# Kernel optimization log

Measured on AMD Instinct MI355X. Metric: run time of the kernel, lower is better.

The kernel has to match this reference:

```python
import jax, jax.numpy as jnp
import numpy as np

EPS = 1e-5
K_GROUP = 8  # k_group_size


def setup_inputs() -> dict:
    key = jax.random.key(0)
    ks = jax.random.split(key, 8)
    C = 384  # encoder_channel
    rn = lambda k, s: (jax.random.normal(k, s, dtype=jnp.float32) * 0.05)
    return {
        "point_groups": jax.random.normal(ks[0], (4, 256, 32, 3), dtype=jnp.float32),
        # first_conv: Conv1d(3,128,1)+BN+ReLU+Conv1d(128,256,1)
        "W1": rn(ks[1], (128, 3)), "b1": jnp.zeros(128, jnp.float32),
        "gamma1": jnp.ones(128, jnp.float32), "beta1": jnp.zeros(128, jnp.float32),
        "W2": rn(ks[2], (256, 128)), "b2": jnp.zeros(256, jnp.float32),
        # second_conv: Conv1d(512,512,1)+BN+ReLU+Conv1d(512,C,1)
        "W3": rn(ks[3], (512, 512)), "b3": jnp.zeros(512, jnp.float32),
        "gamma3": jnp.ones(512, jnp.float32), "beta3": jnp.zeros(512, jnp.float32),
        "W4": rn(ks[4], (C, 512)), "b4": jnp.zeros(C, jnp.float32),
        # K_Norm affine (out_dim = C, matching declared parameter shapes)
        "alpha": jnp.ones((1, 1, 1, C), jnp.float32),
        "beta_aff": jnp.zeros((1, 1, 1, C), jnp.float32),
        # fusion_layer: Conv1d(2C,C,1)+BN+ReLU
        "Wf": rn(ks[5], (C, 2 * C)), "bf": jnp.zeros(C, jnp.float32),
        "gammaf": jnp.ones(C, jnp.float32), "betaf": jnp.zeros(C, jnp.float32),
    }


def _conv1x1(x, W, b):  # x: (B,Cin,L), W: (Cout,Cin)
    return jnp.einsum("bcl,oc->bol", x, W) + b[None, :, None]


def _bn(x, gamma, beta):  # training-mode BatchNorm1d over (batch, length)
    mu = jnp.mean(x, axis=(0, 2), keepdims=True)
    var = jnp.var(x, axis=(0, 2), keepdims=True)
    xh = (x - mu) * jax.lax.rsqrt(var + EPS)
    return xh * gamma[None, :, None] + beta[None, :, None]


def reference(point_groups, W1, b1, gamma1, beta1, W2, b2, W3, b3, gamma3, beta3,
              W4, b4, alpha, beta_aff, Wf, bf, gammaf, betaf):
    bs, g, n, _ = point_groups.shape
    C = W4.shape[0]
    pg = point_groups.reshape(bs * g, n, 3)  # (B', n, 3)

    # first_conv stack
    f = _conv1x1(pg.transpose(0, 2, 1), W1, b1)           # (B',128,n)
    f = jax.nn.relu(_bn(f, gamma1, beta1))
    f = _conv1x1(f, W2, b2)                               # (B',256,n)
    fg = jnp.max(f, axis=2, keepdims=True)                # (B',256,1)
    f = jnp.concatenate([jnp.broadcast_to(fg, f.shape), f], axis=1)  # (B',512,n)

    # second_conv stack
    f = _conv1x1(f, W3, b3)
    f = jax.nn.relu(_bn(f, gamma3, beta3))
    f = _conv1x1(f, W4, b4)                               # (B',C,n)
    feat = f.transpose(0, 2, 1)                           # (B',n,C)

    # KNN within each group (self included, as in KNN(xyz,xyz))
    sq = jnp.sum(pg * pg, axis=-1)                        # (B',n)
    d = sq[:, :, None] + sq[:, None, :] - 2.0 * jnp.einsum("bnc,bmc->bnm", pg, pg)
    _, idx = jax.lax.top_k(-d, K_GROUP)                   # (B',n,K)

    gather = jax.vmap(lambda a, i: a[i])
    knn_x = gather(feat, idx)                             # (B',n,K,C)

    # K_Norm: center-relative normalization by global scalar std (torch.std, ddof=1)
    mean_x = feat[:, :, None, :]
    dx = knn_x - mean_x
    std_x = jnp.std(dx, ddof=1)
    knn_x = dx / (std_x + EPS)
    knn_x = alpha * knn_x + beta_aff                      # (B',n,K,C)

    enhanced = jnp.mean(knn_x, axis=2)                    # mean over K -> (B',n,C)
    enhanced = jnp.mean(enhanced, axis=1)                 # pool over n -> (B',C)

    fg2 = jnp.max(f, axis=2)                              # (B',C)
    fused_in = jnp.concatenate([fg2, enhanced], axis=1)[:, :, None]  # (B',2C,1)
    fused = jax.nn.relu(_bn(_conv1x1(fused_in, Wf, bf), gammaf, betaf))[:, :, 0]
    return fused.reshape(bs, g, C)
```

## Files before the change

kernel.cpp:

```cpp
#include <hip/hip_runtime.h>
#include <math.h>

#define EPS 1e-5f

typedef __attribute__((ext_vector_type(8))) short s16x8;
typedef __attribute__((ext_vector_type(4))) float f32x4;

__device__ __forceinline__ unsigned short f2bf(float x) {
    unsigned u = __float_as_uint(x);
    u += 0x7fffu + ((u >> 16) & 1u);
    return (unsigned short)(u >> 16);
}
__device__ __forceinline__ float bf2f(unsigned short h) {
    return __uint_as_float(((unsigned)h) << 16);
}
__device__ __forceinline__ unsigned long long pack4bf(float a, float b, float c, float d) {
    return (unsigned long long)f2bf(a)
         | ((unsigned long long)f2bf(b) << 16)
         | ((unsigned long long)f2bf(c) << 32)
         | ((unsigned long long)f2bf(d) << 48);
}

template<int CTRL>
__device__ __forceinline__ float dppmov(float x) {
    return __int_as_float(__builtin_amdgcn_update_dpp(
        0, __float_as_int(x), CTRL, 0xF, 0xF, true));
}
__device__ __forceinline__ float red16_sum(float x) {
    x += dppmov<0xB1>(x);
    x += dppmov<0x4E>(x);
    x += dppmov<0x141>(x);
    x += dppmov<0x140>(x);
    return x;
}
__device__ __forceinline__ float red16_max(float x) {
    x = fmaxf(x, dppmov<0xB1>(x));
    x = fmaxf(x, dppmov<0x4E>(x));
    x = fmaxf(x, dppmov<0x141>(x));
    x = fmaxf(x, dppmov<0x140>(x));
    return x;
}

__global__ __launch_bounds__(128) void k1_conv1_knn(
    const float* __restrict__ pg, const float* __restrict__ W1,
    const float* __restrict__ b1,
    const float* __restrict__ W2, const float* __restrict__ W3,
    const float* __restrict__ W4, const float* __restrict__ Wf,
    unsigned short* __restrict__ h1b,
    float* __restrict__ p1sb, float* __restrict__ p1qb,
    int* __restrict__ idxw,
    unsigned short* __restrict__ W2b, unsigned short* __restrict__ W3b,
    unsigned short* __restrict__ W4b, unsigned short* __restrict__ Wfb)
{
    __shared__ float pgs[96];
    __shared__ float sqs[32];
    if (blockIdx.x >= 1024) {
        const int i = (blockIdx.x - 1024) * 128 + threadIdx.x;
        if (i < 32768)  W2b[i] = f2bf(W2[i]);
        if (i < 262144) W3b[i] = f2bf(W3[i]);
        if (i < 196608) W4b[i] = f2bf(W4[i]);
        if (i < 294912) Wfb[i] = f2bf(Wf[i]);
        return;
    }
    const int b = blockIdx.x;
    const int t = threadIdx.x;
    if (t < 96) pgs[t] = pg[b * 96 + t];
    __syncthreads();
    if (t < 32) {
        float x = pgs[t*3+0], y = pgs[t*3+1], z = pgs[t*3+2];
        sqs[t] = x*x + y*y + z*z;
    }
    __syncthreads();
    {
        const float w0 = W1[t*3+0], w1 = W1[t*3+1], w2 = W1[t*3+2];
        const float bb = b1[t];
        float s = 0.f, q = 0.f;
        unsigned short* hcol = h1b + (size_t)b*4096 + t;
        #pragma unroll
        for (int l = 0; l < 32; ++l) {
            float v = fmaf(w2, pgs[l*3+2], fmaf(w1, pgs[l*3+1], fmaf(w0, pgs[l*3+0], bb)));
            hcol[l*128] = f2bf(v); s += v; q += v*v;
        }
        atomicAdd(&p1sb[((b & 7) << 7) + t], s);
        atomicAdd(&p1qb[((b & 7) << 7) + t], q);
    }
    if (t < 32) {
        const float xl = pgs[t*3+0], yl = pgs[t*3+1], zl = pgs[t*3+2];
        const float sql = sqs[t];
        float dist[32];
        #pragma unroll
        for (int m = 0; m < 32; ++m) {
            float dot = xl*pgs[m*3+0] + yl*pgs[m*3+1] + zl*pgs[m*3+2];
            dist[m] = sql + sqs[m] - 2.f*dot;
        }
        unsigned used = 0u;
        int* orow = idxw + b*256 + t*8;
        #pragma unroll
        for (int j = 0; j < 8; ++j) {
            float best = 3.4e38f; int bi = 0;
            #pragma unroll
            for (int m = 0; m < 32; ++m) {
                if (!((used >> m) & 1u) && dist[m] < best) { best = dist[m]; bi = m; }
            }
            used |= (1u << bi);
            orow[j] = bi;
        }
    }
}

__global__ __launch_bounds__(1024, 8) void k3_mfma(
    const unsigned short* __restrict__ h1b,
    const float* __restrict__ gamma1, const float* __restrict__ beta1,
    const float* __restrict__ p1sb, const float* __restrict__ p1qb,
    const unsigned short* __restrict__ W2b, const float* __restrict__ b2,
    const unsigned short* __restrict__ W3b, const float* __restrict__ b3,
    unsigned short* __restrict__ h3b,
    float* __restrict__ p3sb, float* __restrict__ p3qb)
{
    const int g0 = blockIdx.x * 2;
    const int t = threadIdx.x;
    __shared__ __align__(16) unsigned short SB[26128];
    unsigned short* B1  = SB;
    unsigned short* F2  = SB + 8704;
    unsigned short* FGB = SB + 25600;
    __shared__ __align__(16) float sc1s[128], sh1s[128];

    if (t < 128) {
        float S = 0.f, Q = 0.f;
        #pragma unroll
        for (int bb = 0; bb < 8; ++bb) {
            S += p1sb[(bb << 7) + t];
            Q += p1qb[(bb << 7) + t];
        }
        float mu  = S * (1.f/32768.f);
        float var = Q * (1.f/32768.f) - mu*mu;
        float sc  = gamma1[t] * rsqrtf(var + EPS);
        sc1s[t] = sc;
        sh1s[t] = beta1[t] - mu * sc;
    }
    __syncthreads();

    {
        const int l = t >> 4, c0 = (t & 15) * 8;
        const int g = g0 + (l >> 5);
        s16x8 hv = *(const s16x8*)(h1b + (size_t)g*4096 + (l & 31)*128 + c0);
        unsigned short ov[8];
        #pragma unroll
        for (int e = 0; e < 8; ++e) {
            int c = c0 + e;
            float v = fmaxf(fmaf(bf2f((unsigned short)hv[e]), sc1s[c], sh1s[c]), 0.f);
            ov[e] = f2bf(v);
        }
        uint4 o4;
        o4.x = (unsigned)ov[0] | ((unsigned)ov[1] << 16);
        o4.y = (unsigned)ov[2] | ((unsigned)ov[3] << 16);
        o4.z = (unsigned)ov[4] | ((unsigned)ov[5] << 16);
        o4.w = (unsigned)ov[6] | ((unsigned)ov[7] << 16);
        *(uint4*)&B1[l*136 + c0] = o4;
    }
    __syncthreads();

    const int wave = t >> 6;
    const int lane = t & 63;
    const int m    = lane & 15;
    const int quad = lane >> 4;

    f32x4 acc2[4];
    #pragma unroll
    for (int n = 0; n < 4; ++n)
        acc2[n] = (f32x4){0.f, 0.f, 0.f, 0.f};

    #pragma unroll
    for (int kt = 0; kt < 4; ++kt) {
        s16x8 bv[4];
        #pragma unroll
        for (int nt = 0; nt < 4; ++nt)
            bv[nt] = *(const s16x8*)&B1[(nt*16 + m)*136 + kt*32 + quad*8];
        s16x8 av = *(const s16x8*)(W2b + (size_t)(wave*16 + m)*128 + kt*32 + quad*8);
        #pragma unroll
        for (int nt = 0; nt < 4; ++nt)
            acc2[nt] = __builtin_amdgcn_mfma_f32_16x16x32_bf16(av, bv[nt], acc2[nt], 0, 0, 0);
    }

    {
        const int o0 = wave*16 + quad*4;
        #pragma unroll
        for (int r = 0; r < 4; ++r) {
            float bb = b2[o0 + r];
            #pragma unroll
            for (int nt = 0; nt < 4; ++nt) acc2[nt][r] += bb;
        }
        #pragma unroll
        for (int nt = 0; nt < 4; ++nt) {
            const int row = nt*16 + m;
            *(unsigned long long*)&F2[row*264 + o0] =
                pack4bf(acc2[nt][0], acc2[nt][1], acc2[nt][2], acc2[nt][3]);
        }
        float f0[4], f1[4];
        #pragma unroll
        for (int r = 0; r < 4; ++r) {
            f0[r] = red16_max(fmaxf(acc2[0][r], acc2[1][r]));
            f1[r] = red16_max(fmaxf(acc2[2][r], acc2[3][r]));
        }
        if (m == 0) {
            *(unsigned long long*)&FGB[o0]       = pack4bf(f0[0], f0[1], f0[2], f0[3]);
            *(unsigned long long*)&FGB[264 + o0] = pack4bf(f1[0], f1[1], f1[2], f1[3]);
        }
    }
    __syncthreads();

    unsigned short* dst = h3b + (size_t)blockIdx.x * 32768;
    const int binbase = (blockIdx.x & 7) << 9;
    #pragma unroll
    for (int mt = 0; mt < 2; ++mt) {
        const int ot = wave*2 + mt;
        const int o0 = ot*16 + quad*4;

        f32x4 facc = (f32x4){0.f, 0.f, 0.f, 0.f};
        #pragma unroll
        for (int kt = 0; kt < 8; ++kt) {
            s16x8 bg = *(const s16x8*)&FGB[(m & 1)*264 + kt*32 + quad*8];
            s16x8 av = *(const s16x8*)(W3b + (size_t)(ot*16 + m)*512 + kt*32 + quad*8);
            facc = __builtin_amdgcn_mfma_f32_16x16x32_bf16(av, bg, facc, 0, 0, 0);
        }

        f32x4 acc3[4];
        #pragma unroll
        for (int r = 0; r < 4; ++r) {
            float self = facc[r];
            float oth  = dppmov<0xB1>(self);
            float fg_g0 = (m & 1) ? oth : self;
            float fg_g1 = (m & 1) ? self : oth;
            float bb = b3[o0 + r];
            acc3[0][r] = bb + fg_g0;
            acc3[1][r] = bb + fg_g0;
            acc3[2][r] = bb + fg_g1;
            acc3[3][r] = bb + fg_g1;
        }

        #pragma unroll
        for (int kt = 0; kt < 8; ++kt) {
            s16x8 bv[4];
            #pragma unroll
            for (int nt = 0; nt < 4; ++nt)
                bv[nt] = *(const s16x8*)&F2[(nt*16 + m)*264 + kt*32 + quad*8];
            s16x8 av = *(const s16x8*)(W3b + (size_t)(ot*16 + m)*512 + 256 + kt*32 + quad*8);
            #pragma unroll
            for (int nt = 0; nt < 4; ++nt)
                acc3[nt] = __builtin_amdgcn_mfma_f32_16x16x32_bf16(av, bv[nt], acc3[nt], 0, 0, 0);
        }

        float s[4], q[4];
        #pragma unroll
        for (int r = 0; r < 4; ++r) {
            float x0 = acc3[0][r], x1 = acc3[1][r];
            float x2 = acc3[2][r], x3 = acc3[3][r];
            s[r] = (x0 + x1) + (x2 + x3);
            q[r] = (x0*x0 + x1*x1) + (x2*x2 + x3*x3);
        }
        {
            unsigned long long u0 = pack4bf(acc3[0][0], acc3[0][1], acc3[0][2], acc3[0][3]);
            unsigned long long u1 = pack4bf(acc3[1][0], acc3[1][1], acc3[1][2], acc3[1][3]);
            unsigned long long u2 = pack4bf(acc3[2][0], acc3[2][1], acc3[2][2], acc3[2][3]);
            unsigned long long u3 = pack4bf(acc3[3][0], acc3[3][1], acc3[3][2], acc3[3][3]);
            unsigned short* p = dst + (size_t)(ot*64 + lane) * 16;
            *(uint4*)(p)     = make_uint4((unsigned)u0, (unsigned)(u0 >> 32), (unsigned)u1, (unsigned)(u1 >> 32));
            *(uint4*)(p + 8) = make_uint4((unsigned)u2, (unsigned)(u2 >> 32), (unsigned)u3, (unsigned)(u3 >> 32));
        }
        #pragma unroll
        for (int r = 0; r < 4; ++r) {
            s[r] = red16_sum(s[r]);
            q[r] = red16_sum(q[r]);
        }
        if (m == 0) {
            #pragma unroll
            for (int r = 0; r < 4; ++r) {
                atomicAdd(&p3sb[binbase + o0 + r], s[r]);
                atomicAdd(&p3qb[binbase + o0 + r], q[r]);
            }
        }
    }
}

__global__ __launch_bounds__(512, 4) void k5_mfma(
    const unsigned short* __restrict__ h3b,
    const float* __restrict__ gamma3, const float* __restrict__ beta3,
    const float* __restrict__ p3sb, const float* __restrict__ p3qb,
    const unsigned short* __restrict__ W4b, const float* __restrict__ b4,
    const int* __restrict__ idxw,
    float* __restrict__ fg2, float* __restrict__ A,
    float* __restrict__ S1p, float* __restrict__ S2p)
{
    const int g0 = blockIdx.x * 2;
    const int t = threadIdx.x;
    __shared__ __align__(16) unsigned short SB[33280];
    unsigned short* B4 = SB;
    unsigned short* XT = SB;
    unsigned short* Mm = SB + 30720;
    __shared__ __align__(16) float sc3s[512], sh3s[512];
    __shared__ int icnt[2][32];
    __shared__ float r1[2][8], r2[2][8];

    {
        float S = 0.f, Q = 0.f;
        #pragma unroll
        for (int bb = 0; bb < 8; ++bb) {
            S += p3sb[(bb << 9) + t];
            Q += p3qb[(bb << 9) + t];
        }
        float mu  = S * (1.f/32768.f);
        float var = Q * (1.f/32768.f) - mu*mu;
        float sc  = gamma3[t] * rsqrtf(var + EPS);
        sc3s[t] = sc;
        sh3s[t] = beta3[t] - mu * sc;
    }
    if (t < 64) icnt[t >> 5][t & 31] = 0;
    __syncthreads();

    {
        const uint4* src = (const uint4*)(h3b + (size_t)blockIdx.x * 32768);
        for (int i = t; i < 4096; i += 512) {
            uint4 hv = src[i];
            const int flat16 = i >> 1, half = i & 1;
            const int ln = flat16 & 63, m2 = ln & 15, q2 = ln >> 4;
            const int wm = flat16 >> 6;
            const int o0 = wm*16 + q2*4;
            const float4 sc = *(const float4*)&sc3s[o0];
            const float4 sh = *(const float4*)&sh3s[o0];
            const int rowa = (half*2)*16 + m2;
            float a0 = fmaxf(fmaf(bf2f((unsigned short)(hv.x       )), sc.x, sh.x), 0.f);
            float a1 = fmaxf(fmaf(bf2f((unsigned short)(hv.x >> 16 )), sc.y, sh.y), 0.f);
            float a2 = fmaxf(fmaf(bf2f((unsigned short)(hv.y       )), sc.z, sh.z), 0.f);
            float a3 = fmaxf(fmaf(bf2f((unsigned short)(hv.y >> 16 )), sc.w, sh.w), 0.f);
            float b0 = fmaxf(fmaf(bf2f((unsigned short)(hv.z       )), sc.x, sh.x), 0.f);
            float b1 = fmaxf(fmaf(bf2f((unsigned short)(hv.z >> 16 )), sc.y, sh.y), 0.f);
            float b2 = fmaxf(fmaf(bf2f((unsigned short)(hv.w       )), sc.z, sh.z), 0.f);
            float b3 = fmaxf(fmaf(bf2f((unsigned short)(hv.w >> 16 )), sc.w, sh.w), 0.f);
            *(unsigned long long*)&B4[rowa*520 + o0]        = pack4bf(a0, a1, a2, a3);
            *(unsigned long long*)&B4[(rowa + 16)*520 + o0] = pack4bf(b0, b1, b2, b3);
        }
    }
    __syncthreads();

    const int wave = t >> 6;
    const int lane = t & 63;
    const int m    = lane & 15;
    const int quad = lane >> 4;

    f32x4 acc4[3][4];
    #pragma unroll
    for (int mt = 0; mt < 3; ++mt)
        #pragma unroll
        for (int n = 0; n < 4; ++n)
            acc4[mt][n] = (f32x4){0.f, 0.f, 0.f, 0.f};

    #pragma unroll 4
    for (int kt = 0; kt < 16; ++kt) {
        s16x8 bv[4];
        #pragma unroll
        for (int nt = 0; nt < 4; ++nt)
            bv[nt] = *(const s16x8*)&B4[(nt*16 + m)*520 + kt*32 + quad*8];
        #pragma unroll
        for (int mt = 0; mt < 3; ++mt) {
            s16x8 av = *(const s16x8*)(W4b + (size_t)(wave*48 + mt*16 + m)*512 + kt*32 + quad*8);
            #pragma unroll
            for (int nt = 0; nt < 4; ++nt)
                acc4[mt][nt] = __builtin_amdgcn_mfma_f32_16x16x32_bf16(av, bv[nt], acc4[mt][nt], 0, 0, 0);
        }
    }

    #pragma unroll
    for (int mt = 0; mt < 3; ++mt) {
        const int o0 = wave*48 + mt*16 + quad*4;
        float f0[4], f1[4];
        #pragma unroll
        for (int r = 0; r < 4; ++r) {
            float bb = b4[o0 + r];
            #pragma unroll
            for (int nt = 0; nt < 4; ++nt) acc4[mt][nt][r] += bb;
            f0[r] = red16_max(fmaxf(acc4[mt][0][r], acc4[mt][1][r]));
            f1[r] = red16_max(fmaxf(acc4[mt][2][r], acc4[mt][3][r]));
        }
        if (m == 0) {
            #pragma unroll
            for (int r = 0; r < 4; ++r) {
                fg2[(size_t)g0*384 + o0 + r]     = f0[r];
                fg2[(size_t)(g0+1)*384 + o0 + r] = f1[r];
            }
        }
    }
    __syncthreads();

    #pragma unroll
    for (int mt = 0; mt < 3; ++mt) {
        const int o0 = wave*48 + mt*16 + quad*4;
        #pragma unroll
        for (int nt = 0; nt < 4; ++nt) {
            const int g = nt >> 1;
            const int l = (nt & 1)*16 + m;
            unsigned short* xg = XT + g*15360;
            #pragma unroll
            for (int r = 0; r < 4; ++r)
                xg[(o0 + r)*40 + l] = f2bf(acc4[mt][nt][r]);
        }
    }
    if (t < 64) {
        const int g = t >> 5, l = t & 31;
        uint4 z = make_uint4(0u, 0u, 0u, 0u);
        #pragma unroll
        for (int i = 0; i < 5; ++i)
            *(uint4*)&Mm[g*1280 + l*40 + i*8] = z;
    }
    __syncthreads();

    if (t < 64) {
        const int g = t >> 5, l = t & 31;
        const int* ip = idxw + (size_t)(g0 + g)*256 + l*8;
        #pragma unroll
        for (int j = 0; j < 8; ++j) {
            int ix = ip[j];
            Mm[g*1280 + l*40 + ix] = 0x3F80;
            atomicAdd(&icnt[g][ix], 1);
        }
    }
    __syncthreads();

    float s1loc[2] = {0.f, 0.f}, s2loc[2] = {0.f, 0.f};
    #pragma unroll
    for (int g = 0; g < 2; ++g) {
        const float c0 = (float)icnt[g][m];
        const float c1 = (float)icnt[g][m + 16];
        const float w0 = c0 - 8.f, u0 = c0 + 8.f;
        const float w1 = c1 - 8.f, u1 = c1 + 8.f;
        #pragma unroll
        for (int mt = 0; mt < 3; ++mt) {
            const int o0 = wave*48 + mt*16 + quad*4;
            float Ap[4];
            #pragma unroll
            for (int r = 0; r < 4; ++r) {
                const float x0 = acc4[mt][g*2 + 0][r];
                const float x1 = acc4[mt][g*2 + 1][r];
                Ap[r] = w0*x0 + w1*x1;
                s1loc[g] += Ap[r];
                s2loc[g] += u0*x0*x0 + u1*x1*x1;
            }
            #pragma unroll
            for (int r = 0; r < 4; ++r)
                Ap[r] = red16_sum(Ap[r]);
            if (m == 0) {
                #pragma unroll
                for (int r = 0; r < 4; ++r)
                    A[(size_t)(g0 + g)*384 + o0 + r] = Ap[r];
            }
        }
    }

    #pragma unroll
    for (int g = 0; g < 2; ++g) {
        const unsigned short* xg = XT + g*15360;
        float cross = 0.f;
        #pragma unroll
        for (int lt = 0; lt < 2; ++lt) {
            s16x8 af = *(const s16x8*)&Mm[g*1280 + (lt*16 + m)*40 + quad*8];
            #pragma unroll
            for (int i = 0; i < 3; ++i) {
                const int oc = (wave*3 + i)*16 + m;
                s16x8 bfv = *(const s16x8*)&xg[oc*40 + quad*8];
                f32x4 sa = __builtin_amdgcn_mfma_f32_16x16x32_bf16(
                    af, bfv, (f32x4){0.f, 0.f, 0.f, 0.f}, 0, 0, 0);
                #pragma unroll
                for (int r = 0; r < 4; ++r) {
                    const int lp = lt*16 + quad*4 + r;
                    cross = fmaf(bf2f(xg[oc*40 + lp]), sa[r], cross);
                }
            }
        }
        s2loc[g] -= 2.f * cross;
    }

    #pragma unroll
    for (int g = 0; g < 2; ++g) {
        float sA = s1loc[g], sQ = s2loc[g];
        #pragma unroll
        for (int off = 32; off > 0; off >>= 1) {
            sA += __shfl_down(sA, off, 64);
            sQ += __shfl_down(sQ, off, 64);
        }
        if (lane == 0) { r1[g][wave] = sA; r2[g][wave] = sQ; }
    }
    __syncthreads();
    if (t < 2) {
        float S = 0.f, Q = 0.f;
        #pragma unroll
        for (int w = 0; w < 8; ++w) { S += r1[t][w]; Q += r2[t][w]; }
        S1p[g0 + t] = S;
        S2p[g0 + t] = Q;
    }
}

__global__ __launch_bounds__(384) void k7_fused(
    const float* __restrict__ fg2, const float* __restrict__ A,
    const float* __restrict__ alpha, const float* __restrict__ beta_aff,
    const float* __restrict__ S1p, const float* __restrict__ S2p,
    const unsigned short* __restrict__ Wfb, const float* __restrict__ bf,
    float* __restrict__ hf, float* __restrict__ pfs, float* __restrict__ pfq)
{
    const int blk    = blockIdx.x;
    const int slice  = blk >> 2;
    const int msplit = blk & 3;
    const int g0     = slice * 16;
    const int obase  = msplit * 96;
    const int t = threadIdx.x;
    __shared__ __align__(16) char smem[24832];
    unsigned short* xfb = (unsigned short*)smem;
    float* OTf = (float*)smem;
    __shared__ double rs[6], rq[6];
    __shared__ float stdsh;

    {
        double s = 0.0, q = 0.0;
        for (int i = t; i < 1024; i += 384) { s += (double)S1p[i]; q += (double)S2p[i]; }
        #pragma unroll
        for (int off = 32; off > 0; off >>= 1) {
            s += __shfl_down(s, off, 64);
            q += __shfl_down(q, off, 64);
        }
        if ((t & 63) == 0) { rs[t >> 6] = s; rq[t >> 6] = q; }
        __syncthreads();
        if (t == 0) {
            double S = 0.0, Q = 0.0;
            #pragma unroll
            for (int w = 0; w < 6; ++w) { S += rs[w]; Q += rq[w]; }
            const double N = 1024.0 * 32.0 * 8.0 * 384.0;
            double var = (Q - S*S/N) / (N - 1.0);
            stdsh = (float)sqrt(var);
        }
        __syncthreads();
    }
    const float inv = 1.f / (256.f * (stdsh + EPS));

    for (int i = t; i < 16*96; i += 384) {
        const int row = i / 96, c8 = (i % 96) * 8;
        const int g = g0 + row;
        float e[8];
        if (c8 < 384) {
            const float4* s0 = (const float4*)(fg2 + (size_t)g*384 + c8);
            float4 v0 = s0[0], v1 = s0[1];
            e[0]=v0.x; e[1]=v0.y; e[2]=v0.z; e[3]=v0.w;
            e[4]=v1.x; e[5]=v1.y; e[6]=v1.z; e[7]=v1.w;
        } else {
            const int cc = c8 - 384;
            const float4* s0 = (const float4*)(A + (size_t)g*384 + cc);
            float4 v0 = s0[0], v1 = s0[1];
            float av[8] = {v0.x,v0.y,v0.z,v0.w,v1.x,v1.y,v1.z,v1.w};
            #pragma unroll
            for (int j = 0; j < 8; ++j)
                e[j] = fmaf(alpha[cc+j] * inv, av[j], beta_aff[cc+j]);
        }
        uint4 o4;
        o4.x = (unsigned)f2bf(e[0]) | ((unsigned)f2bf(e[1]) << 16);
        o4.y = (unsigned)f2bf(e[2]) | ((unsigned)f2bf(e[3]) << 16);
        o4.z = (unsigned)f2bf(e[4]) | ((unsigned)f2bf(e[5]) << 16);
        o4.w = (unsigned)f2bf(e[6]) | ((unsigned)f2bf(e[7]) << 16);
        *(uint4*)&xfb[row*776 + c8] = o4;
    }
    __syncthreads();

    const int wave = t >> 6;
    const int lane = t & 63;
    const int m    = lane & 15;
    const int quad = lane >> 4;

    f32x4 acc = (f32x4){0.f, 0.f, 0.f, 0.f};
    #pragma unroll 4
    for (int kt = 0; kt < 24; ++kt) {
        s16x8 bv = *(const s16x8*)&xfb[m*776 + kt*32 + quad*8];
        s16x8 av = *(const s16x8*)(Wfb + (size_t)(obase + wave*16 + m)*768 + kt*32 + quad*8);
        acc = __builtin_amdgcn_mfma_f32_16x16x32_bf16(av, bv, acc, 0, 0, 0);
    }

    {
        const int o0 = obase + wave*16 + quad*4;
        float s[4], q[4];
        #pragma unroll
        for (int r = 0; r < 4; ++r) {
            acc[r] += bf[o0 + r];
            s[r] = red16_sum(acc[r]);
            q[r] = red16_sum(acc[r]*acc[r]);
        }
        if (m == 0) {
            #pragma unroll
            for (int r = 0; r < 4; ++r) {
                pfs[(size_t)slice*384 + o0 + r] = s[r];
                pfq[(size_t)slice*384 + o0 + r] = q[r];
            }
        }
    }
    __syncthreads();

    {
        const int lo0 = wave*16 + quad*4;
        #pragma unroll
        for (int r = 0; r < 4; ++r)
            OTf[m*100 + lo0 + r] = acc[r];
    }
    __syncthreads();

    {
        const int grp = t / 24, c4 = t % 24;
        float4 v = *(const float4*)&OTf[grp*100 + c4*4];
        *(float4*)(hf + (size_t)(g0 + grp)*384 + obase + c4*4) = v;
    }
}

__global__ __launch_bounds__(384) void k9_out(
    const float* __restrict__ hf,
    const float* __restrict__ pfs, const float* __restrict__ pfq,
    const float* __restrict__ gammaf, const float* __restrict__ betaf,
    float* __restrict__ out)
{
    const int blk = blockIdx.x, t = threadIdx.x;
    float S = 0.f, Q = 0.f;
    #pragma unroll 8
    for (int i = 0; i < 64; ++i) {
        S += pfs[(size_t)i*384 + t];
        Q += pfq[(size_t)i*384 + t];
    }
    const float mu  = S * (1.f/1024.f);
    const float var = Q * (1.f/1024.f) - mu*mu;
    const float sc  = gammaf[t] * rsqrtf(var + EPS);
    const float sh  = betaf[t] - mu * sc;
    const size_t base = (size_t)blk * 8 * 384;
    #pragma unroll
    for (int g = 0; g < 8; ++g) {
        float v = fmaf(hf[base + g*384 + t], sc, sh);
        out[base + g*384 + t] = fmaxf(v, 0.f);
    }
}

extern "C" void kernel_launch(void* const* d_in, const int* in_sizes, int n_in,
                              void* d_out, int out_size, void* d_ws, size_t ws_size,
                              hipStream_t stream) {
    const float* pg      = (const float*)d_in[0];
    const float* W1      = (const float*)d_in[1];
    const float* b1      = (const float*)d_in[2];
    const float* gamma1  = (const float*)d_in[3];
    const float* beta1   = (const float*)d_in[4];
    const float* W2      = (const float*)d_in[5];
    const float* b2      = (const float*)d_in[6];
    const float* W3      = (const float*)d_in[7];
    const float* b3      = (const float*)d_in[8];
    const float* gamma3  = (const float*)d_in[9];
    const float* beta3   = (const float*)d_in[10];
    const float* W4      = (const float*)d_in[11];
    const float* b4      = (const float*)d_in[12];
    const float* alpha   = (const float*)d_in[13];
    const float* beta_af = (const float*)d_in[14];
    const float* Wf      = (const float*)d_in[15];
    const float* bf      = (const float*)d_in[16];
    const float* gammaf  = (const float*)d_in[17];
    const float* betaf   = (const float*)d_in[18];
    float* out = (float*)d_out;

    float* w = (float*)d_ws;
    unsigned short* h1b = (unsigned short*)w; w += 1024*4096/2;
    unsigned short* h3b = (unsigned short*)w; w += 1024*16384/2;
    unsigned short* W2b = (unsigned short*)w; w += 32768/2;
    unsigned short* W3b = (unsigned short*)w; w += 262144/2;
    unsigned short* W4b = (unsigned short*)w; w += 196608/2;
    unsigned short* Wfb = (unsigned short*)w; w += 294912/2;
    float* hf     = w;  w += 1024*384;
    float* fg2    = w;  w += 1024*384;
    float* A      = w;  w += 1024*384;
    float* p1sb   = w;  w += 8*128;
    float* p1qb   = w;  w += 8*128;
    float* p3sb   = w;  w += 8*512;
    float* p3qb   = w;  w += 8*512;
    float* pfs    = w;  w += 64*384;
    float* pfq    = w;  w += 64*384;
    float* S1p    = w;  w += 1024;
    float* S2p    = w;  w += 1024;
    int*   idxw   = (int*)w;  w += 1024*256;

    hipMemsetAsync(p1sb, 0, (8*128*2 + 8*512*2) * sizeof(float), stream);
    hipLaunchKernelGGL(k1_conv1_knn, dim3(1024 + 2304), dim3(128), 0, stream,
                       pg, W1, b1, W2, W3, W4, Wf,
                       h1b, p1sb, p1qb, idxw, W2b, W3b, W4b, Wfb);
    hipLaunchKernelGGL(k3_mfma, dim3(512), dim3(1024), 0, stream,
                       h1b, gamma1, beta1, p1sb, p1qb, W2b, b2, W3b, b3,
                       h3b, p3sb, p3qb);
    hipLaunchKernelGGL(k5_mfma, dim3(512), dim3(512), 0, stream,
                       h3b, gamma3, beta3, p3sb, p3qb, W4b, b4, idxw,
                       fg2, A, S1p, S2p);
    hipLaunchKernelGGL(k7_fused, dim3(256), dim3(384), 0, stream,
                       fg2, A, alpha, beta_af, S1p, S2p, Wfb, bf, hf, pfs, pfq);
    hipLaunchKernelGGL(k9_out, dim3(128), dim3(384), 0, stream,
                       hf, pfs, pfq, gammaf, betaf, out);
}
```

Before: 195.5 us.

## Derive BN1 statistics from point moments and recompute conv1 inside k3

The first conv is linear in xyz, so its per-channel sum and sum of squares are now derived from nine per-group coordinate moments instead of materialising the bf16 h1 activation and atomically accumulating stats. k3 reloads the raw points and W1 and recomputes conv1 on the fly, so the h1b round-trip through global memory goes away. The hipMemsetAsync is replaced by zeroing inside the prep kernel, and the p3 stat bins are widened from 8 to 16 to reduce atomic contention. The risk is cancellation in the moment-based variance formula, and k3 does a little extra arithmetic.

```diff
diff --git a/kernel.cpp b/kernel.cpp
--- a/kernel.cpp
+++ b/kernel.cpp
@@ -41,25 +41,30 @@
     return x;
 }
 
-__global__ __launch_bounds__(128) void k1_conv1_knn(
-    const float* __restrict__ pg, const float* __restrict__ W1,
-    const float* __restrict__ b1,
+__global__ __launch_bounds__(128) void k1_prep(
+    const float* __restrict__ pg,
     const float* __restrict__ W2, const float* __restrict__ W3,
     const float* __restrict__ W4, const float* __restrict__ Wf,
-    unsigned short* __restrict__ h1b,
-    float* __restrict__ p1sb, float* __restrict__ p1qb,
-    int* __restrict__ idxw,
+    float* __restrict__ mom, int* __restrict__ idxw,
     unsigned short* __restrict__ W2b, unsigned short* __restrict__ W3b,
-    unsigned short* __restrict__ W4b, unsigned short* __restrict__ Wfb)
+    unsigned short* __restrict__ W4b, unsigned short* __restrict__ Wfb,
+    float* __restrict__ p3sb, float* __restrict__ p3qb)
 {
     __shared__ float pgs[96];
     __shared__ float sqs[32];
     if (blockIdx.x >= 1024) {
-        const int i = (blockIdx.x - 1024) * 128 + threadIdx.x;
+        const int wb = blockIdx.x - 1024;
+        const int i = wb * 128 + threadIdx.x;
         if (i < 32768)  W2b[i] = f2bf(W2[i]);
         if (i < 262144) W3b[i] = f2bf(W3[i]);
         if (i < 196608) W4b[i] = f2bf(W4[i]);
         if (i < 294912) Wfb[i] = f2bf(Wf[i]);
+        if (wb < 16) {
+            for (int j = threadIdx.x; j < 512; j += 128) {
+                p3sb[wb*512 + j] = 0.f;
+                p3qb[wb*512 + j] = 0.f;
+            }
+        }
         return;
     }
     const int b = blockIdx.x;
@@ -71,26 +76,24 @@
         sqs[t] = x*x + y*y + z*z;
     }
     __syncthreads();
-    {
-        const float w0 = W1[t*3+0], w1 = W1[t*3+1], w2 = W1[t*3+2];
-        const float bb = b1[t];
-        float s = 0.f, q = 0.f;
-        unsigned short* hcol = h1b + (size_t)b*4096 + t;
-        #pragma unroll
-        for (int l = 0; l < 32; ++l) {
-            float v = fmaf(w2, pgs[l*3+2], fmaf(w1, pgs[l*3+1], fmaf(w0, pgs[l*3+0], bb)));
-            hcol[l*128] = f2bf(v); s += v; q += v*v;
-        }
-        atomicAdd(&p1sb[((b & 7) << 7) + t], s);
-        atomicAdd(&p1qb[((b & 7) << 7) + t], q);
-    }
     if (t < 32) {
-        const float xl = pgs[t*3+0], yl = pgs[t*3+1], zl = pgs[t*3+2];
+        const float x = pgs[t*3+0], y = pgs[t*3+1], z = pgs[t*3+2];
+        float v[9] = {x, y, z, x*x, x*y, x*z, y*y, y*z, z*z};
+        #pragma unroll
+        for (int off = 16; off > 0; off >>= 1)
+            #pragma unroll
+            for (int j = 0; j < 9; ++j)
+                v[j] += __shfl_down(v[j], off, 32);
+        if (t == 0) {
+            #pragma unroll
+            for (int j = 0; j < 9; ++j)
+                mom[j*1024 + b] = v[j];
+        }
         const float sql = sqs[t];
         float dist[32];
         #pragma unroll
         for (int m = 0; m < 32; ++m) {
-            float dot = xl*pgs[m*3+0] + yl*pgs[m*3+1] + zl*pgs[m*3+2];
+            float dot = x*pgs[m*3+0] + y*pgs[m*3+1] + z*pgs[m*3+2];
             dist[m] = sql + sqs[m] - 2.f*dot;
         }
         unsigned used = 0u;
@@ -109,9 +112,10 @@
 }
 
 __global__ __launch_bounds__(1024, 8) void k3_mfma(
-    const unsigned short* __restrict__ h1b,
+    const float* __restrict__ pg,
+    const float* __restrict__ W1, const float* __restrict__ b1,
     const float* __restrict__ gamma1, const float* __restrict__ beta1,
-    const float* __restrict__ p1sb, const float* __restrict__ p1qb,
+    const float* __restrict__ mom,
     const unsigned short* __restrict__ W2b, const float* __restrict__ b2,
     const unsigned short* __restrict__ W3b, const float* __restrict__ b3,
     unsigned short* __restrict__ h3b,
@@ -124,17 +128,43 @@
     unsigned short* F2  = SB + 8704;
     unsigned short* FGB = SB + 25600;
     __shared__ __align__(16) float sc1s[128], sh1s[128];
+    __shared__ __align__(16) float W1s[384], b1s[128];
+    __shared__ __align__(16) float pgs3[192];
+    __shared__ float momS[9];
+
+    if (t < 192) pgs3[t] = pg[g0*96 + t];
+    if (t < 384) W1s[t] = W1[t];
+    if (t < 128) b1s[t] = b1[t];
+    {
+        const int wv = t >> 6, ln = t & 63;
+        if (wv < 9) {
+            float s = 0.f;
+            #pragma unroll
+            for (int i = 0; i < 16; ++i)
+                s += mom[wv*1024 + ln + 64*i];
+            #pragma unroll
+            for (int off = 32; off > 0; off >>= 1)
+                s += __shfl_down(s, off, 64);
+            if (ln == 0) momS[wv] = s;
+        }
+    }
+    __syncthreads();
 
     if (t < 128) {
-        float S = 0.f, Q = 0.f;
-        #pragma unroll
-        for (int bb = 0; bb < 8; ++bb) {
-            S += p1sb[(bb << 7) + t];
-            Q += p1qb[(bb << 7) + t];
-        }
-        float mu  = S * (1.f/32768.f);
-        float var = Q * (1.f/32768.f) - mu*mu;
-        float sc  = gamma1[t] * rsqrtf(var + EPS);
+        const float Sx = momS[0], Sy = momS[1], Sz = momS[2];
+        const float Sxx = momS[3], Sxy = momS[4], Sxz = momS[5];
+        const float Syy = momS[6], Syz = momS[7], Szz = momS[8];
+        const float w0 = W1s[t*3+0], w1 = W1s[t*3+1], w2 = W1s[t*3+2];
+        const float bb = b1s[t];
+        const float N = 32768.f;
+        const float wd = w0*Sx + w1*Sy + w2*Sz;
+        const float S = wd + N*bb;
+        const float Q = w0*w0*Sxx + w1*w1*Syy + w2*w2*Szz
+                      + 2.f*(w0*w1*Sxy + w0*w2*Sxz + w1*w2*Syz)
+                      + 2.f*bb*wd + N*bb*bb;
+        const float mu  = S * (1.f/32768.f);
+        const float var = Q * (1.f/32768.f) - mu*mu;
+        const float sc  = gamma1[t] * rsqrtf(var + EPS);
         sc1s[t] = sc;
         sh1s[t] = beta1[t] - mu * sc;
     }
@@ -142,14 +172,14 @@
 
     {
         const int l = t >> 4, c0 = (t & 15) * 8;
-        const int g = g0 + (l >> 5);
-        s16x8 hv = *(const s16x8*)(h1b + (size_t)g*4096 + (l & 31)*128 + c0);
+        const float px = pgs3[l*3+0], py = pgs3[l*3+1], pz = pgs3[l*3+2];
         unsigned short ov[8];
         #pragma unroll
         for (int e = 0; e < 8; ++e) {
-            int c = c0 + e;
-            float v = fmaxf(fmaf(bf2f((unsigned short)hv[e]), sc1s[c], sh1s[c]), 0.f);
-            ov[e] = f2bf(v);
+            const int c = c0 + e;
+            float v = fmaf(W1s[c*3+2], pz, fmaf(W1s[c*3+1], py, fmaf(W1s[c*3+0], px, b1s[c])));
+            float val = fmaxf(fmaf(v, sc1s[c], sh1s[c]), 0.f);
+            ov[e] = f2bf(val);
         }
         uint4 o4;
         o4.x = (unsigned)ov[0] | ((unsigned)ov[1] << 16);
@@ -210,7 +240,7 @@
     __syncthreads();
 
     unsigned short* dst = h3b + (size_t)blockIdx.x * 32768;
-    const int binbase = (blockIdx.x & 7) << 9;
+    const int binbase = (blockIdx.x & 15) * 512;
     #pragma unroll
     for (int mt = 0; mt < 2; ++mt) {
         const int ot = wave*2 + mt;
@@ -304,9 +334,9 @@
     {
         float S = 0.f, Q = 0.f;
         #pragma unroll
-        for (int bb = 0; bb < 8; ++bb) {
-            S += p3sb[(bb << 9) + t];
-            Q += p3qb[(bb << 9) + t];
+        for (int bb = 0; bb < 16; ++bb) {
+            S += p3sb[bb*512 + t];
+            Q += p3qb[bb*512 + t];
         }
         float mu  = S * (1.f/32768.f);
         float var = Q * (1.f/32768.f) - mu*mu;
@@ -663,7 +693,6 @@
     float* out = (float*)d_out;
 
     float* w = (float*)d_ws;
-    unsigned short* h1b = (unsigned short*)w; w += 1024*4096/2;
     unsigned short* h3b = (unsigned short*)w; w += 1024*16384/2;
     unsigned short* W2b = (unsigned short*)w; w += 32768/2;
     unsigned short* W3b = (unsigned short*)w; w += 262144/2;
@@ -672,22 +701,20 @@
     float* hf     = w;  w += 1024*384;
     float* fg2    = w;  w += 1024*384;
     float* A      = w;  w += 1024*384;
-    float* p1sb   = w;  w += 8*128;
-    float* p1qb   = w;  w += 8*128;
-    float* p3sb   = w;  w += 8*512;
-    float* p3qb   = w;  w += 8*512;
+    float* mom    = w;  w += 12*1024;
+    float* p3sb   = w;  w += 16*512;
+    float* p3qb   = w;  w += 16*512;
     float* pfs    = w;  w += 64*384;
     float* pfq    = w;  w += 64*384;
     float* S1p    = w;  w += 1024;
     float* S2p    = w;  w += 1024;
     int*   idxw   = (int*)w;  w += 1024*256;
 
-    hipMemsetAsync(p1sb, 0, (8*128*2 + 8*512*2) * sizeof(float), stream);
-    hipLaunchKernelGGL(k1_conv1_knn, dim3(1024 + 2304), dim3(128), 0, stream,
-                       pg, W1, b1, W2, W3, W4, Wf,
-                       h1b, p1sb, p1qb, idxw, W2b, W3b, W4b, Wfb);
+    hipLaunchKernelGGL(k1_prep, dim3(1024 + 2304), dim3(128), 0, stream,
+                       pg, W2, W3, W4, Wf,
+                       mom, idxw, W2b, W3b, W4b, Wfb, p3sb, p3qb);
     hipLaunchKernelGGL(k3_mfma, dim3(512), dim3(1024), 0, stream,
-                       h1b, gamma1, beta1, p1sb, p1qb, W2b, b2, W3b, b3,
+                       pg, W1, b1, gamma1, beta1, mom, W2b, b2, W3b, b3,
                        h3b, p3sb, p3qb);
     hipLaunchKernelGGL(k5_mfma, dim3(512), dim3(512), 0, stream,
                        h3b, gamma3, beta3, p3sb, p3qb, W4b, b4, idxw,
```

After: 195.3 us. Within noise of the previous version (-0.1%).
